# Kernel tuning notes

Measured on AMD Instinct MI355X. Metric: run time of the kernel, lower is better.

Reference implementation:

```python
import jax, jax.numpy as jnp
import numpy as np

B, R, L, K, E, H, V, QV = 256, 6, 10, 49, 300, 512, 2001, 10000


def _lstm_dir(x, Wih, Whh, bih, bhh):
    # x: [N, L, E]; returns final hidden state [N, H] (PyTorch gate order i,f,g,o)
    N = x.shape[0]
    Hd = Whh.shape[1]
    b = bih + bhh

    def step(carry, xt):
        h, c = carry
        gates = xt @ Wih.T + h @ Whh.T + b
        i, f, g, o = jnp.split(gates, 4, axis=-1)
        c = jax.nn.sigmoid(f) * c + jax.nn.sigmoid(i) * jnp.tanh(g)
        h = jax.nn.sigmoid(o) * jnp.tanh(c)
        return (h, c), None

    init = (jnp.zeros((N, Hd), x.dtype), jnp.zeros((N, Hd), x.dtype))
    (h, _), _ = jax.lax.scan(step, init, jnp.swapaxes(x, 0, 1))
    return h


def setup_inputs() -> dict:
    key = jax.random.key(0)
    ks = jax.random.split(key, 40)
    s = 0.02
    d = {}
    d['img'] = jax.random.normal(ks[0], (B * R, K, H), jnp.float32)
    d['role_qs'] = jax.random.randint(ks[1], (B, R, L), 0, QV, jnp.int64)
    d['qword_emb'] = jax.random.normal(ks[2], (QV, E), jnp.float32) * s
    d['lstm_Wih_f'] = jax.random.normal(ks[3], (4 * H, E), jnp.float32) * s
    d['lstm_Whh_f'] = jax.random.normal(ks[4], (4 * H, H), jnp.float32) * s
    d['lstm_bih_f'] = jnp.zeros((4 * H,), jnp.float32)
    d['lstm_bhh_f'] = jnp.zeros((4 * H,), jnp.float32)
    d['lstm_Wih_b'] = jax.random.normal(ks[5], (4 * H, E), jnp.float32) * s
    d['lstm_Whh_b'] = jax.random.normal(ks[6], (4 * H, H), jnp.float32) * s
    d['lstm_bih_b'] = jnp.zeros((4 * H,), jnp.float32)
    d['lstm_bhh_b'] = jnp.zeros((4 * H,), jnp.float32)
    d['proj_W'] = jax.random.normal(ks[7], (H, 2 * H), jnp.float32) * s
    d['proj_b'] = jnp.zeros((H,), jnp.float32)
    d['vatt_vW'] = jax.random.normal(ks[8], (H, H), jnp.float32) * s
    d['vatt_vb'] = jnp.zeros((H,), jnp.float32)
    d['vatt_qW'] = jax.random.normal(ks[9], (H, H), jnp.float32) * s
    d['vatt_qb'] = jnp.zeros((H,), jnp.float32)
    d['vatt_oW'] = jax.random.normal(ks[10], (1, H), jnp.float32) * s
    d['vatt_ob'] = jnp.zeros((1,), jnp.float32)
    d['qnet_W'] = jax.random.normal(ks[11], (H, H), jnp.float32) * s
    d['qnet_b'] = jnp.zeros((H,), jnp.float32)
    d['vnet_W'] = jax.random.normal(ks[12], (H, H), jnp.float32) * s
    d['vnet_b'] = jnp.zeros((H,), jnp.float32)
    d['cls_W1'] = jax.random.normal(ks[13], (2 * H, H), jnp.float32) * s
    d['cls_b1'] = jnp.zeros((2 * H,), jnp.float32)
    d['cls_W2'] = jax.random.normal(ks[14], (V, 2 * H), jnp.float32) * s
    d['cls_b2'] = jnp.zeros((V,), jnp.float32)
    d['g0_W'] = jax.random.normal(ks[15], (H, 2 * H), jnp.float32) * s
    d['g0_b'] = jnp.zeros((H,), jnp.float32)
    d['g1_W'] = jax.random.normal(ks[16], (H, H), jnp.float32) * s
    d['g1_b'] = jnp.zeros((H,), jnp.float32)
    d['g2_W'] = jax.random.normal(ks[17], (H, H), jnp.float32) * s
    d['g2_b'] = jnp.zeros((H,), jnp.float32)
    d['g3_W'] = jax.random.normal(ks[18], (H, H), jnp.float32) * s
    d['g3_b'] = jnp.zeros((H,), jnp.float32)
    d['f0_W'] = jax.random.normal(ks[19], (H, H), jnp.float32) * s
    d['f0_b'] = jnp.zeros((H,), jnp.float32)
    d['f1_W'] = jax.random.normal(ks[20], (H, H), jnp.float32) * s
    d['f1_b'] = jnp.zeros((H,), jnp.float32)
    return d


def _forward(img, qword_emb,
             lstm_Wih_f, lstm_Whh_f, lstm_bih_f, lstm_bhh_f,
             lstm_Wih_b, lstm_Whh_b, lstm_bih_b, lstm_bhh_b,
             proj_W, proj_b, vatt_vW, vatt_vb, vatt_qW, vatt_qb, vatt_oW, vatt_ob,
             qnet_W, qnet_b, vnet_W, vnet_b, cls_W1, cls_b1, cls_W2, cls_b2,
             g0_W, g0_b, g1_W, g1_b, g2_W, g2_b, g3_W, g3_b,
             f0_W, f0_b, f1_W, f1_b, role_qs):
    relu = jax.nn.relu
    bsz, roles = role_qs.shape[0], role_qs.shape[1]
    toks = role_qs.reshape(-1, role_qs.shape[-1])          # [B*R, L]
    w_emb = qword_emb[toks]                                 # [B*R, L, E]
    # bidirectional LSTM final hidden states
    h_f = _lstm_dir(w_emb, lstm_Wih_f, lstm_Whh_f, lstm_bih_f, lstm_bhh_f)
    h_b = _lstm_dir(w_emb[:, ::-1, :], lstm_Wih_b, lstm_Whh_b, lstm_bih_b, lstm_bhh_b)
    q_emb = jnp.concatenate([h_f, h_b], axis=-1) @ proj_W.T + proj_b   # [B*R, H]
    # top-down attention over image regions
    v_proj = relu(img @ vatt_vW.T + vatt_vb)                # [B*R, K, H]
    q_proj = relu(q_emb @ vatt_qW.T + vatt_qb)              # [B*R, H]
    att_logits = (v_proj * q_proj[:, None, :]) @ vatt_oW.T + vatt_ob  # [B*R, K, 1]
    att = jax.nn.softmax(att_logits, axis=1)
    v_emb = jnp.sum(att * img, axis=1)                      # [B*R, H]
    # joint representation + answer classifier
    q_repr = relu(q_emb @ qnet_W.T + qnet_b)
    v_repr = relu(v_emb @ vnet_W.T + vnet_b)
    joint_repr = q_repr * v_repr                            # [B*R, H]
    logits = relu(joint_repr @ cls_W1.T + cls_b1) @ cls_W2.T + cls_b2  # [B*R, V]
    # relation network over pairwise role representations
    jr = joint_repr.reshape(bsz, roles, -1)                 # [B, R, H]
    r1 = jnp.broadcast_to(jr[:, None, :, :], (bsz, roles, roles, jr.shape[-1]))
    r2 = jnp.broadcast_to(jr[:, :, None, :], (bsz, roles, roles, jr.shape[-1]))
    cat = jnp.concatenate([r1, r2], axis=-1).reshape(-1, 2 * jr.shape[-1])  # [B*R*R, 2H]
    g = relu(cat @ g0_W.T + g0_b)
    g = relu(g @ g1_W.T + g1_b)
    g = relu(g @ g2_W.T + g2_b)
    g = relu(g @ g3_W.T + g3_b)
    g = g.reshape(bsz, roles * roles, -1).sum(axis=1)       # [B, H]
    rec = relu(g @ f0_W.T + f0_b) @ f1_W.T + f1_b           # [B, H]
    rec = rec / jnp.sqrt(jnp.sum(rec * rec, axis=1, keepdims=True))  # l2norm
    return logits, rec


def reference(img, role_qs, qword_emb,
              lstm_Wih_f, lstm_Whh_f, lstm_bih_f, lstm_bhh_f,
              lstm_Wih_b, lstm_Whh_b, lstm_bih_b, lstm_bhh_b,
              proj_W, proj_b, vatt_vW, vatt_vb, vatt_qW, vatt_qb, vatt_oW, vatt_ob,
              qnet_W, qnet_b, vnet_W, vnet_b, cls_W1, cls_b1, cls_W2, cls_b2,
              g0_W, g0_b, g1_W, g1_b, g2_W, g2_b, g3_W, g3_b,
              f0_W, f0_b, f1_W, f1_b):
    return _forward(img, qword_emb,
                    lstm_Wih_f, lstm_Whh_f, lstm_bih_f, lstm_bhh_f,
                    lstm_Wih_b, lstm_Whh_b, lstm_bih_b, lstm_bhh_b,
                    proj_W, proj_b, vatt_vW, vatt_vb, vatt_qW, vatt_qb, vatt_oW, vatt_ob,
                    qnet_W, qnet_b, vnet_W, vnet_b, cls_W1, cls_b1, cls_W2, cls_b2,
                    g0_W, g0_b, g1_W, g1_b, g2_W, g2_b, g3_W, g3_b,
                    f0_W, f0_b, f1_W, f1_b, role_qs)
```

## Files before the change

### kernel.cpp

```cpp
#include <hip/hip_runtime.h>
#include <hip/hip_bf16.h>
#include <math.h>

typedef __attribute__((ext_vector_type(8))) short short8;
typedef __attribute__((ext_vector_type(4))) float f32x4;

#define KTILE 32
#define LSTR 40
#define LSTR64 72

__device__ __forceinline__ short8 cvt8(const float* x) {
    short8 r;
#pragma unroll
    for (int i = 0; i < 8; ++i) {
        __hip_bfloat16 b = __float2bfloat16(x[i]);
        r[i] = *reinterpret_cast<const short*>(&b);
    }
    return r;
}
__device__ __forceinline__ float bf2f(short s) {
    unsigned int u = ((unsigned int)(unsigned short)s) << 16;
    return __uint_as_float(u);
}

template<int BM>
__global__ __launch_bounds__(256)
void mfma_gemm_t(const float* __restrict__ A1f, int lda1, int k1,
                 const short* __restrict__ W1, int ldw1,
                 const float* __restrict__ A2f, int lda2, int k2,
                 const short* __restrict__ W2, int ldw2,
                 const float* __restrict__ bias1,
                 const float* __restrict__ mulvec, const float* __restrict__ mul,
                 float* __restrict__ C, int ldc, int M, int N,
                 int do_relu, int mode, int abits, int c_bf16)
{
    __shared__ short sA[2][BM][LSTR];
    __shared__ short sB[2][64][LSTR];
    __shared__ float sred[BM][2];
    constexpr int MF = BM / 32;

    const int tid = threadIdx.x;
    int m0, n0, ch8 = 0;
    if (mode == 1) {
        const int xcd = blockIdx.x & 7;
        const int gi = xcd * 588 + (blockIdx.x >> 3);
        m0 = (gi >> 3) << 7;
        ch8 = gi & 7;
        n0 = ch8 << 6;
    } else {
        m0 = blockIdx.y * BM;
        n0 = blockIdx.x << 6;
    }
    const short* A1b = (const short*)A1f;
    const short* A2b = (const short*)A2f;
    const int Ktot = k1 + k2;
// ... 134 lines not shown
                }
            }
        }
    } else {
#pragma unroll
        for (int m = 0; m < MF; ++m) {
#pragma unroll
            for (int j = 0; j < 4; ++j) {
                const int rloc = wr + (m << 4) + (lh << 2) + j;
                const int r = m0 + rloc;
                const size_t sqbase = (size_t)(r / 49) * ldc;
                float s = 0.f;
#pragma unroll
                for (int n = 0; n < 2; ++n) {
                    const int c = n0 + wc + (n << 4) + l15;
                    float v = acc[m][n][j] + bias1[c];
                    v = fmaxf(v, 0.f);
                    s += v * mul[sqbase + c];
                }
                s += __shfl_xor(s, 1, 64);
                s += __shfl_xor(s, 2, 64);
                s += __shfl_xor(s, 4, 64);
                s += __shfl_xor(s, 8, 64);
                if (l15 == 0) sred[rloc][wc >> 5] = s;
            }
        }
        __syncthreads();
        if (tid < BM)
            C[(size_t)(m0 + tid) * 8 + ch8] = sred[tid][0] + sred[tid][1];
    }
}

__global__ __launch_bounds__(256)
void mfma_gemm64_kernel(const float* __restrict__ A1f, int lda1, int k1,
                        const short* __restrict__ W1, int ldw1,
                        const float* __restrict__ A2f, int lda2, int k2,
                        const short* __restrict__ W2, int ldw2,
                        const float* __restrict__ bias1,
                        const float* __restrict__ mulvec, const float* __restrict__ mul,
                        float* __restrict__ C, int ldc, int M, int N,
                        int do_relu, int abits, int c_bf16)
{
    __shared__ short sA[2][64][LSTR64];
    __shared__ short sB[2][64][LSTR64];
    const int tid = threadIdx.x;
    const int m0 = blockIdx.y << 6, n0 = blockIdx.x << 6;
    const short* A1b = (const short*)A1f;
    const short* A2b = (const short*)A2f;
    const int Ktot = k1 + k2;
    const int nt = (Ktot + 63) >> 6;
    const int lane = tid & 63, wave = tid >> 6;
    const int wr = (wave >> 1) << 5, wc = (wave & 1) << 5;
    const int l15 = lane & 15, lh = lane >> 4;
    const int srow = tid >> 2, skq = (tid & 3) << 4;
    const int rgA = min(m0 + srow, M - 1);
    const int ngW = min(n0 + srow, N - 1);

    f32x4 acc[2][2];
#pragma unroll
    for (int m = 0; m < 2; ++m)
#pragma unroll
        for (int n = 0; n < 2; ++n) acc[m][n] = (f32x4){0.f, 0.f, 0.f, 0.f};

    short8 aS0, aS1, wS0, wS1;
    auto loadA = [&](int t) {
        const int k0 = (t << 6) + skq;
// ... 118 lines not shown
                 const float* __restrict__ vnet, const float* __restrict__ cls1,
                 const float* __restrict__ cls2, const float* __restrict__ g0,
                 const float* __restrict__ g1, const float* __restrict__ g2,
                 const float* __restrict__ g3, const float* __restrict__ f0,
                 const float* __restrict__ f1, short* __restrict__ dst)
{
    size_t idx = ((size_t)blockIdx.x * 256 + threadIdx.x) * 8;
    if (idx >= 5981184) return;
    const float* s;
    if (idx < 524288) s = proj + idx;
    else if (idx < 786432) s = qW + (idx - 524288);
    else if (idx < 1048576) s = vW + (idx - 786432);
    else if (idx < 1310720) s = qnet + (idx - 1048576);
    else if (idx < 1572864) s = vnet + (idx - 1310720);
    else if (idx < 2097152) s = cls1 + (idx - 1572864);
    else if (idx < 4146176) s = cls2 + (idx - 2097152);
    else if (idx < 4670464) {
        size_t li = idx - 4146176;
        int c = (int)(li >> 9), k = (int)(li & 511);
        s = (c < 512) ? g0 + (size_t)c * 1024 + k
                      : g0 + (size_t)(c - 512) * 1024 + 512 + k;
    }
    else if (idx < 4932608) s = g1 + (idx - 4670464);
    else if (idx < 5194752) s = g2 + (idx - 4932608);
    else if (idx < 5456896) s = g3 + (idx - 5194752);
    else if (idx < 5719040) s = f0 + (idx - 5456896);
    else s = f1 + (idx - 5719040);
    float4 a = *(const float4*)s, b = *(const float4*)(s + 4);
    float t[8] = {a.x, a.y, a.z, a.w, b.x, b.y, b.z, b.w};
    *(short8*)(dst + idx) = cvt8(t);
}

__global__ __launch_bounds__(256)
void lstm_reorder_kernel(const float* __restrict__ Wih, const float* __restrict__ Whh,
                         const float* __restrict__ bih, const float* __restrict__ bhh,
                         short* __restrict__ Wbf, float* __restrict__ bias_perm)
{
    int id = blockIdx.x * 256 + threadIdx.x;
    int c = id >> 9, k = id & 511;
    int src = (c & 3) * 512 + (c >> 2);
    {
        __hip_bfloat16 b = __float2bfloat16(Whh[(size_t)src * 512 + k]);
        Wbf[(size_t)c * 832 + k] = *(short*)&b;
    }
    if (k < 300) {
        __hip_bfloat16 b = __float2bfloat16(Wih[(size_t)src * 300 + k]);
        Wbf[(size_t)c * 832 + 512 + k] = *(short*)&b;
    } else if (k < 320) {
        Wbf[(size_t)c * 832 + 512 + k] = 0;
    }
    if (k == 0) bias_perm[c] = bih[src] + bhh[src];
}

__global__ __launch_bounds__(256)
void lstm_step4_kernel(const short* __restrict__ hF_in, const short* __restrict__ hB_in,
                       const short* __restrict__ WbfF, const short* __restrict__ WbfB,
                       const float* __restrict__ biasF, const float* __restrict__ biasB,
                       const float* __restrict__ emb, const int* __restrict__ toks,
                       int tF, int tB, int first,
                       short* __restrict__ hF_out, short* __restrict__ hB_out,
                       float* __restrict__ cF, float* __restrict__ cB)
{
    __shared__ short sA[2][64][LSTR64];
    __shared__ short sB[2][64][LSTR64];
    const int dir = blockIdx.z;
    const short* h_in = dir ? hB_in : hF_in;
    const short* Wbf  = dir ? WbfB : WbfF;
    const float* bias_perm = dir ? biasB : biasF;
    short* h_out  = dir ? hB_out : hF_out;
    float* cstate = dir ? cB : cF;
    const int tt = dir ? tB : tF;

    const int tid = threadIdx.x;
    const int m0 = blockIdx.y << 6;
    const int n0 = blockIdx.x << 6;
    const int lane = tid & 63, wave = tid >> 6;
    const int wr = (wave >> 1) << 5, wc = (wave & 1) << 5;
    const int l15 = lane & 15, lh = lane >> 4;
    const int srow = tid >> 2, skq = (tid & 3) << 4;
    const int rgA = m0 + srow;
    const int ngW = n0 + srow;
    const int nt = 13;
    const int arow = toks[rgA * 10 + tt];

    f32x4 acc[2][2];
#pragma unroll
    for (int m = 0; m < 2; ++m)
#pragma unroll
        for (int n = 0; n < 2; ++n) acc[m][n] = (f32x4){0.f, 0.f, 0.f, 0.f};

    short8 aS0, aS1, wS0, wS1;
    auto loadA = [&](int t) {
        const int k0 = (t << 6) + skq;
        if (k0 + 16 <= 512) {
            if (first) { short8 z = {0,0,0,0,0,0,0,0}; aS0 = z; aS1 = z; }
            else {
                const short* p = h_in + (size_t)rgA * 512 + k0;
                aS0 = *(const short8*)p; aS1 = *(const short8*)(p + 8);
            }
        } else if (k0 >= 512 && k0 + 16 <= 812) {
            const float* p = emb + (size_t)arow * 300 + (k0 - 512);
            float4 v0 = *(const float4*)p, v1 = *(const float4*)(p + 4);
            float4 v2 = *(const float4*)(p + 8), v3 = *(const float4*)(p + 12);
            float t0[8] = {v0.x, v0.y, v0.z, v0.w, v1.x, v1.y, v1.z, v1.w};
            float t1[8] = {v2.x, v2.y, v2.z, v2.w, v3.x, v3.y, v3.z, v3.w};
            aS0 = cvt8(t0); aS1 = cvt8(t1);
        } else {
            float tmp[16];
#pragma unroll
            for (int e = 0; e < 16; ++e) {
                const int kg = k0 + e;
                float v = 0.f;
                if (kg < 512) v = first ? 0.f : bf2f(h_in[(size_t)rgA * 512 + kg]);
                else if (kg < 812) v = emb[(size_t)arow * 300 + (kg - 512)];
                tmp[e] = v;
            }
            aS0 = cvt8(tmp); aS1 = cvt8(tmp + 8);
        }
    };
    auto loadW = [&](int t) {
        const short* p = Wbf + (size_t)ngW * 832 + (t << 6) + skq;
        wS0 = *(const short8*)p; wS1 = *(const short8*)(p + 8);
    };
    auto writeS = [&](int buf) {
        *(short8*)&sA[buf][srow][skq] = aS0;
        *(short8*)&sA[buf][srow][skq + 8] = aS1;
        *(short8*)&sB[buf][srow][skq] = wS0;
        *(short8*)&sB[buf][srow][skq + 8] = wS1;
    };

    loadA(0); loadW(0); writeS(0);
    __syncthreads();
    for (int t = 0; t < nt; ++t) {
        const int cur = t & 1;
        if (t + 1 < nt) { loadA(t + 1); loadW(t + 1); }
#pragma unroll
        for (int kk = 0; kk < 2; ++kk) {
            short8 af[2], bfv[2];
#pragma unroll
            for (int m = 0; m < 2; ++m)
                af[m] = *(const short8*)&sA[cur][wr + (m << 4) + l15][(kk << 5) + (lh << 3)];
#pragma unroll
            for (int n = 0; n < 2; ++n)
                bfv[n] = *(const short8*)&sB[cur][wc + (n << 4) + l15][(kk << 5) + (lh << 3)];
#pragma unroll
            for (int m = 0; m < 2; ++m)
#pragma unroll
                for (int n = 0; n < 2; ++n)
                    acc[m][n] = __builtin_amdgcn_mfma_f32_16x16x32_bf16(af[m], bfv[n], acc[m][n], 0, 0, 0);
        }
        if (t + 1 < nt) writeS(cur ^ 1);
        __syncthreads();
    }

#pragma unroll
    for (int n = 0; n < 2; ++n) {
        const int ccol = n0 + wc + (n << 4) + l15;
        const float bb = bias_perm[ccol];
        const int u = ccol >> 2;
#pragma unroll
        for (int m = 0; m < 2; ++m) {
#pragma unroll
            for (int j = 0; j < 4; ++j) {
                const int r = m0 + wr + (m << 4) + (lh << 2) + j;
                float v = acc[m][n][j] + bb;
                const int base = lane & ~3;
                float gi = __shfl(v, base, 64);
                float gf = __shfl(v, base | 1, 64);
                float gg = __shfl(v, base | 2, 64);
                float go = __shfl(v, base | 3, 64);
                if ((lane & 3) == 0) {
                    float si = 1.f / (1.f + expf(-gi));
                    float sf = 1.f / (1.f + expf(-gf));
                    float so = 1.f / (1.f + expf(-go));
                    size_t idx = ((size_t)r << 9) + u;
                    float cold = first ? 0.f : cstate[idx];
                    float cv = sf * cold + si * tanhf(gg);
                    cstate[idx] = cv;
                    float hv = so * tanhf(cv);
                    __hip_bfloat16 b = __float2bfloat16(hv);
                    h_out[idx] = *(short*)&b;
                }
            }
        }
    }
}

__global__ __launch_bounds__(256)
void imgcvt_kernel(const float* __restrict__ img, short* __restrict__ out)
{
    size_t i = ((size_t)blockIdx.x * 256 + threadIdx.x) * 8;
    float4 a = *(const float4*)(img + i), b = *(const float4*)(img + i + 4);
    float t[8] = {a.x, a.y, a.z, a.w, b.x, b.y, b.z, b.w};
    *(short8*)(out + i) = cvt8(t);
}

__global__ __launch_bounds__(256)
void attn_vemb_kernel(const float* __restrict__ partial, const float* __restrict__ img,
                      const short* __restrict__ imgb, float* __restrict__ v_emb)
{
    __shared__ float satt[49];
    const int n = blockIdx.x;
    const int tid = threadIdx.x;
    if (tid < 64) {
        float v = -1e30f;
        if (tid < 49) {
            const float* pp = partial + ((size_t)n * 49 + tid) * 8;
            v = ((pp[0] + pp[1]) + (pp[2] + pp[3])) + ((pp[4] + pp[5]) + (pp[6] + pp[7]));
        }
        float m = v;
#pragma unroll
        for (int off = 32; off; off >>= 1) m = fmaxf(m, __shfl_xor(m, off, 64));
        float e = (tid < 49) ? expf(v - m) : 0.f;
        float s = e;
// ... 103 lines not shown
    const float* cls_W2 = (const float*)d_in[25];
    const float* cls_b2 = (const float*)d_in[26];
    const float* g0_W   = (const float*)d_in[27];
    const float* g0_b   = (const float*)d_in[28];
    const float* g1_W   = (const float*)d_in[29];
    const float* g1_b   = (const float*)d_in[30];
    const float* g2_W   = (const float*)d_in[31];
    const float* g2_b   = (const float*)d_in[32];
    const float* g3_W   = (const float*)d_in[33];
    const float* g3_b   = (const float*)d_in[34];
    const float* f0_W   = (const float*)d_in[35];
    const float* f0_b   = (const float*)d_in[36];
    const float* f1_W   = (const float*)d_in[37];
    const float* f1_b   = (const float*)d_in[38];

    float* out_logits = (float*)d_out;
    float* out_rec    = (float*)d_out + 1536 * 2001;

    const size_t FB = 786432;
    float* zone = (float*)d_ws;
    float* gA    = zone;
    float* gB    = zone + 4718592;
    float* hid1  = zone + 9437184;
    float* PQb   = zone + 11010048;
    float* gsumb = zone + 12582912;
    float* f0o   = zone + 12713984;
    float* rectb = zone + 12845056;
    float* p = zone + 12976128;
    auto alloc = [&](size_t nf) { float* q = p; p += nf; return q; };
    float* hP0   = alloc(FB);
    float* hP2   = alloc(FB);
    float* joint = alloc(FB);
    float* partial = alloc(602112);
    short* WbfF  = (short*)alloc(851968);
    short* WbfB  = (short*)alloc(851968);
    float* biasF = alloc(2048);
    float* biasB = alloc(2048);
    const size_t TOPF = 17645568;
    short* wb = (short*)(zone + TOPF);
    short* projbf = wb;
    short* qWbf   = wb + 524288;
    short* vWbf   = wb + 786432;
    short* qnetbf = wb + 1048576;
    short* vnetbf = wb + 1310720;
    short* cls1bf = wb + 1572864;
    short* cls2bf = wb + 2097152;
    short* wpqbf  = wb + 4146176;
    short* g1bf   = wb + 4670464;
    short* g2bf   = wb + 4932608;
    short* g3bf   = wb + 5194752;
    short* f0bf   = wb + 5456896;
    short* f1bf   = wb + 5719040;
    const size_t WEND = TOPF + 2990592;
    const size_t IMGBF = 19267584;
    const bool useimgbf = ws_size >= (WEND + IMGBF) * sizeof(float);
    short* imgbf = (short*)(zone + WEND);
    short* hP1 = (short*)gA;
    short* hP3 = (short*)(gA + FB);
    float* cF  = gA + 2 * FB;
    float* cB  = gA + 3 * FB;
    float* q_emb  = PQb;
    float* swq    = hid1;
    float* q_repr = gA;
    float* v_emb  = gA + FB;

    auto gemm = [&](const float* A1, int lda1, int k1, const short* W1, int ldw1,
                    const float* A2, int lda2, int k2, const short* W2, int ldw2,
                    const float* b1, const float* mv, const float* mulp,
                    float* Cp, int ldc, int M, int N, int relu, int abits, int cbf) {
        if (M >= 4096) {
            dim3 g((N + 63) / 64, (M + 127) / 128);
            hipLaunchKernelGGL(HIP_KERNEL_NAME(mfma_gemm_t<128>), g, dim3(256), 0, stream,
                               A1, lda1, k1, W1, ldw1, A2, lda2, k2, W2, ldw2,
                               b1, mv, mulp, Cp, ldc, M, N, relu, 0, abits, cbf);
        } else {
            dim3 g((N + 63) / 64, (M + 63) / 64);
            hipLaunchKernelGGL(mfma_gemm64_kernel, g, dim3(256), 0, stream,
                               A1, lda1, k1, W1, ldw1, A2, lda2, k2, W2, ldw2,
                               b1, mv, mulp, Cp, ldc, M, N, relu, abits, cbf);
        }
    };

    const int NR = 1536;
    hipLaunchKernelGGL(lstm_reorder_kernel, dim3(4096), dim3(256), 0, stream,
                       Wih_f, Whh_f, bih_f, bhh_f, WbfF, biasF);
    hipLaunchKernelGGL(lstm_reorder_kernel, dim3(4096), dim3(256), 0, stream,
                       Wih_b, Whh_b, bih_b, bhh_b, WbfB, biasB);
    hipLaunchKernelGGL(wcvt_kernel, dim3(2921), dim3(256), 0, stream,
                       proj_W, vatt_qW, vatt_vW, qnet_W, vnet_W, cls_W1, cls_W2,
                       g0_W, g1_W, g2_W, g3_W, f0_W, f1_W, wb);
    if (useimgbf)
        hipLaunchKernelGGL(imgcvt_kernel, dim3(18816), dim3(256), 0, stream, img, imgbf);
    {
        short *fi = (short*)hP0, *fo = hP1, *bi = (short*)hP2, *bo = hP3;
        for (int t = 0; t < 10; ++t) {
            hipLaunchKernelGGL(lstm_step4_kernel, dim3(32, 24, 2), dim3(256), 0, stream,
                               fi, bi, WbfF, WbfB, biasF, biasB, qword, toks, t, 9 - t,
                               (t == 0) ? 1 : 0, fo, bo, cF, cB);
            short* tmp = fi; fi = fo; fo = tmp;
            tmp = bi; bi = bo; bo = tmp;
        }
    }

    gemm(hP0, 512, 512, projbf, 1024, hP2, 512, 512, projbf + 512, 1024,
         proj_b, nullptr, nullptr, q_emb, 512, NR, 512, 0, 3, 1);
    gemm(q_emb, 512, 512, qWbf, 512, nullptr, 0, 0, nullptr, 0,
         vatt_qb, vatt_oW, nullptr, swq, 512, NR, 512, 1, 1, 0);
    hipLaunchKernelGGL(HIP_KERNEL_NAME(mfma_gemm_t<128>), dim3(4704), dim3(256), 0, stream,
                       useimgbf ? (const float*)imgbf : img, 512, 512, vWbf, 512,
                       (const float*)nullptr, 0, 0, (const short*)nullptr, 0,
                       vatt_vb, (const float*)nullptr, swq,
                       partial, 512, 75264, 512, 0, 1, useimgbf ? 1 : 0, 0);
    hipLaunchKernelGGL(attn_vemb_kernel, dim3(1536), dim3(256), 0, stream,
                       partial, img, useimgbf ? imgbf : (const short*)nullptr, v_emb);
    gemm(q_emb, 512, 512, qnetbf, 512, nullptr, 0, 0, nullptr, 0,
         qnet_b, nullptr, nullptr, q_repr, 512, NR, 512, 1, 1, 0);
    gemm(v_emb, 512, 512, vnetbf, 512, nullptr, 0, 0, nullptr, 0,
         vnet_b, nullptr, q_repr, joint, 512, NR, 512, 1, 0, 1);
    gemm(joint, 512, 512, cls1bf, 512, nullptr, 0, 0, nullptr, 0,
         cls_b1, nullptr, nullptr, hid1, 1024, NR, 1024, 1, 1, 1);
    gemm(hid1, 1024, 1024, cls2bf, 1024, nullptr, 0, 0, nullptr, 0,
         cls_b2, nullptr, nullptr, out_logits, 2001, NR, 2001, 0, 1, 0);
    gemm(joint, 512, 512, wpqbf, 512, nullptr, 0, 0, nullptr, 0,
         nullptr, nullptr, nullptr, PQb, 1024, NR, 1024, 0, 1, 0);
    hipLaunchKernelGGL(g0build_kernel, dim3(18432), dim3(256), 0, stream,
                       PQb, g0_b, (short*)gA);
    gemm(gA, 512, 512, g1bf, 512, nullptr, 0, 0, nullptr, 0,
         g1_b, nullptr, nullptr, gB, 512, 9216, 512, 1, 1, 1);
    gemm(gB, 512, 512, g2bf, 512, nullptr, 0, 0, nullptr, 0,
         g2_b, nullptr, nullptr, gA, 512, 9216, 512, 1, 1, 1);
    gemm(gA, 512, 512, g3bf, 512, nullptr, 0, 0, nullptr, 0,
         g3_b, nullptr, nullptr, gB, 512, 9216, 512, 1, 1, 1);
    hipLaunchKernelGGL(gsum_kernel, dim3(512), dim3(256), 0, stream, (const short*)gB, gsumb);
    gemm(gsumb, 512, 512, f0bf, 512, nullptr, 0, 0, nullptr, 0,
         f0_b, nullptr, nullptr, f0o, 512, 256, 512, 1, 0, 0);
    gemm(f0o, 512, 512, f1bf, 512, nullptr, 0, 0, nullptr, 0,
         f1_b, nullptr, nullptr, rectb, 512, 256, 512, 0, 0, 0);
    hipLaunchKernelGGL(l2norm_kernel, dim3(256), dim3(256), 0, stream, rectb, out_rec);
}
```

Measured before the change: 828.5 us.

## Pre-swizzle LSTM weights into MFMA fragment layout and drop LDS staging

The LSTM weight reorder kernel now writes bf16 weights in the exact per-lane MFMA B-fragment order, so each wave reads its operand with one contiguous 16-byte load per lane. The step kernel drops the shared-memory double buffer and the barriers and loads A fragments (hidden state and embeddings) straight from global memory into registers. On the first step it skips the hidden-state half of K entirely. The trade-off is the loss of LDS reuse across waves: A rows are now loaded by two waves and W by two waves, and there is no software prefetch to hide global latency.

```diff
diff --git a/kernel.cpp b/kernel.cpp
--- a/kernel.cpp
+++ b/kernel.cpp
@@ -405,56 +405,57 @@
 }
 
 __global__ __launch_bounds__(256)
-void lstm_reorder_kernel(const float* __restrict__ Wih, const float* __restrict__ Whh,
-                         const float* __restrict__ bih, const float* __restrict__ bhh,
-                         short* __restrict__ Wbf, float* __restrict__ bias_perm)
+void lstm_reorder2_kernel(const float* __restrict__ Wih, const float* __restrict__ Whh,
+                          const float* __restrict__ bih, const float* __restrict__ bhh,
+                          short* __restrict__ WP, float* __restrict__ bias_perm)
 {
     int id = blockIdx.x * 256 + threadIdx.x;
-    int c = id >> 9, k = id & 511;
+    int c = id / 832, k = id % 832;
     int src = (c & 3) * 512 + (c >> 2);
-    {
-        __hip_bfloat16 b = __float2bfloat16(Whh[(size_t)src * 512 + k]);
-        Wbf[(size_t)c * 832 + k] = *(short*)&b;
-    }
-    if (k < 300) {
-        __hip_bfloat16 b = __float2bfloat16(Wih[(size_t)src * 300 + k]);
-        Wbf[(size_t)c * 832 + 512 + k] = *(short*)&b;
-    } else if (k < 320) {
-        Wbf[(size_t)c * 832 + 512 + k] = 0;
-    }
+    float v = 0.f;
+    if (k < 512) v = Whh[(size_t)src * 512 + k];
+    else if (k < 812) v = Wih[(size_t)src * 300 + (k - 512)];
+    __hip_bfloat16 b = __float2bfloat16(v);
+    const int cb = c >> 6, rem = c & 63;
+    const int wc2 = rem >> 5, n2 = (rem >> 4) & 1, l15 = rem & 15;
+    const int t = k >> 5, kk = k & 31;
+    const int lane = ((kk >> 3) << 4) + l15;
+    const int s = (cb * 2 + wc2) * 52 + t * 2 + n2;
+    WP[(size_t)s * 512 + lane * 8 + (kk & 7)] = *(short*)&b;
     if (k == 0) bias_perm[c] = bih[src] + bhh[src];
 }
 
 __global__ __launch_bounds__(256)
-void lstm_step4_kernel(const short* __restrict__ hF_in, const short* __restrict__ hB_in,
-                       const short* __restrict__ WbfF, const short* __restrict__ WbfB,
+void lstm_step5_kernel(const short* __restrict__ hF_in, const short* __restrict__ hB_in,
+                       const short* __restrict__ WPF, const short* __restrict__ WPB,
                        const float* __restrict__ biasF, const float* __restrict__ biasB,
                        const float* __restrict__ emb, const int* __restrict__ toks,
                        int tF, int tB, int first,
                        short* __restrict__ hF_out, short* __restrict__ hB_out,
                        float* __restrict__ cF, float* __restrict__ cB)
 {
-    __shared__ short sA[2][64][LSTR64];
-    __shared__ short sB[2][64][LSTR64];
     const int dir = blockIdx.z;
     const short* h_in = dir ? hB_in : hF_in;
-    const short* Wbf  = dir ? WbfB : WbfF;
+    const short* WP   = dir ? WPB : WPF;
     const float* bias_perm = dir ? biasB : biasF;
     short* h_out  = dir ? hB_out : hF_out;
     float* cstate = dir ? cB : cF;
     const int tt = dir ? tB : tF;
 
     const int tid = threadIdx.x;
+    const int lane = tid & 63, wave = tid >> 6;
+    const int cb = blockIdx.x;
     const int m0 = blockIdx.y << 6;
-    const int n0 = blockIdx.x << 6;
-    const int lane = tid & 63, wave = tid >> 6;
-    const int wr = (wave >> 1) << 5, wc = (wave & 1) << 5;
+    const int wr = (wave >> 1) << 5;
+    const int wc2 = wave & 1;
+    const int wc = wc2 << 5;
+    const int n0 = cb << 6;
     const int l15 = lane & 15, lh = lane >> 4;
-    const int srow = tid >> 2, skq = (tid & 3) << 4;
-    const int rgA = m0 + srow;
-    const int ngW = n0 + srow;
-    const int nt = 13;
-    const int arow = toks[rgA * 10 + tt];
+
+    const int row0 = m0 + wr + l15;
+    const int row1 = row0 + 16;
+    const int arow0 = toks[row0 * 10 + tt];
+    const int arow1 = toks[row1 * 10 + tt];
 
     f32x4 acc[2][2];
 #pragma unroll
@@ -462,68 +463,48 @@
 #pragma unroll
         for (int n = 0; n < 2; ++n) acc[m][n] = (f32x4){0.f, 0.f, 0.f, 0.f};
 
-    short8 aS0, aS1, wS0, wS1;
-    auto loadA = [&](int t) {
-        const int k0 = (t << 6) + skq;
-        if (k0 + 16 <= 512) {
-            if (first) { short8 z = {0,0,0,0,0,0,0,0}; aS0 = z; aS1 = z; }
-            else {
-                const short* p = h_in + (size_t)rgA * 512 + k0;
-                aS0 = *(const short8*)p; aS1 = *(const short8*)(p + 8);
-            }
-        } else if (k0 >= 512 && k0 + 16 <= 812) {
-            const float* p = emb + (size_t)arow * 300 + (k0 - 512);
-            float4 v0 = *(const float4*)p, v1 = *(const float4*)(p + 4);
-            float4 v2 = *(const float4*)(p + 8), v3 = *(const float4*)(p + 12);
-            float t0[8] = {v0.x, v0.y, v0.z, v0.w, v1.x, v1.y, v1.z, v1.w};
-            float t1[8] = {v2.x, v2.y, v2.z, v2.w, v3.x, v3.y, v3.z, v3.w};
-            aS0 = cvt8(t0); aS1 = cvt8(t1);
+    const short* wp = WP + ((size_t)(cb * 2 + wc2) * 52) * 512 + (lane << 3);
+
+    if (!first) {
+        for (int t = 0; t < 16; ++t) {
+            short8 af0 = *(const short8*)(h_in + (size_t)row0 * 512 + (t << 5) + (lh << 3));
+            short8 af1 = *(const short8*)(h_in + (size_t)row1 * 512 + (t << 5) + (lh << 3));
+            short8 bf0 = *(const short8*)(wp + (size_t)(t * 2) * 512);
+            short8 bf1 = *(const short8*)(wp + (size_t)(t * 2 + 1) * 512);
+            acc[0][0] = __builtin_amdgcn_mfma_f32_16x16x32_bf16(af0, bf0, acc[0][0], 0, 0, 0);
+            acc[0][1] = __builtin_amdgcn_mfma_f32_16x16x32_bf16(af0, bf1, acc[0][1], 0, 0, 0);
+            acc[1][0] = __builtin_amdgcn_mfma_f32_16x16x32_bf16(af1, bf0, acc[1][0], 0, 0, 0);
+            acc[1][1] = __builtin_amdgcn_mfma_f32_16x16x32_bf16(af1, bf1, acc[1][1], 0, 0, 0);
+        }
+    }
+    for (int t = 16; t < 26; ++t) {
+        const int c0 = (t << 5) + (lh << 3) - 512;
+        short8 af0, af1;
+        if (c0 + 8 <= 300) {
+            const float* p0 = emb + (size_t)arow0 * 300 + c0;
+            float4 u0 = *(const float4*)p0, u1 = *(const float4*)(p0 + 4);
+            float t0[8] = {u0.x, u0.y, u0.z, u0.w, u1.x, u1.y, u1.z, u1.w};
+            af0 = cvt8(t0);
+            const float* p1 = emb + (size_t)arow1 * 300 + c0;
+            float4 v0 = *(const float4*)p1, v1 = *(const float4*)(p1 + 4);
+            float t1[8] = {v0.x, v0.y, v0.z, v0.w, v1.x, v1.y, v1.z, v1.w};
+            af1 = cvt8(t1);
         } else {
-            float tmp[16];
-#pragma unroll
-            for (int e = 0; e < 16; ++e) {
-                const int kg = k0 + e;
-                float v = 0.f;
-                if (kg < 512) v = first ? 0.f : bf2f(h_in[(size_t)rgA * 512 + kg]);
-                else if (kg < 812) v = emb[(size_t)arow * 300 + (kg - 512)];
-                tmp[e] = v;
-            }
-            aS0 = cvt8(tmp); aS1 = cvt8(tmp + 8);
-        }
-    };
-    auto loadW = [&](int t) {
-        const short* p = Wbf + (size_t)ngW * 832 + (t << 6) + skq;
-        wS0 = *(const short8*)p; wS1 = *(const short8*)(p + 8);
-    };
-    auto writeS = [&](int buf) {
-        *(short8*)&sA[buf][srow][skq] = aS0;
-        *(short8*)&sA[buf][srow][skq + 8] = aS1;
-        *(short8*)&sB[buf][srow][skq] = wS0;
-        *(short8*)&sB[buf][srow][skq + 8] = wS1;
-    };
-
-    loadA(0); loadW(0); writeS(0);
-    __syncthreads();
-    for (int t = 0; t < nt; ++t) {
-        const int cur = t & 1;
-        if (t + 1 < nt) { loadA(t + 1); loadW(t + 1); }
-#pragma unroll
-        for (int kk = 0; kk < 2; ++kk) {
-            short8 af[2], bfv[2];
-#pragma unroll
-            for (int m = 0; m < 2; ++m)
-                af[m] = *(const short8*)&sA[cur][wr + (m << 4) + l15][(kk << 5) + (lh << 3)];
-#pragma unroll
-            for (int n = 0; n < 2; ++n)
-                bfv[n] = *(const short8*)&sB[cur][wc + (n << 4) + l15][(kk << 5) + (lh << 3)];
-#pragma unroll
-            for (int m = 0; m < 2; ++m)
-#pragma unroll
-                for (int n = 0; n < 2; ++n)
-                    acc[m][n] = __builtin_amdgcn_mfma_f32_16x16x32_bf16(af[m], bfv[n], acc[m][n], 0, 0, 0);
-        }
-        if (t + 1 < nt) writeS(cur ^ 1);
-        __syncthreads();
+            float t0[8], t1[8];
+#pragma unroll
+            for (int e = 0; e < 8; ++e) {
+                const int kg = c0 + e;
+                t0[e] = (kg < 300) ? emb[(size_t)arow0 * 300 + kg] : 0.f;
+                t1[e] = (kg < 300) ? emb[(size_t)arow1 * 300 + kg] : 0.f;
+            }
+            af0 = cvt8(t0); af1 = cvt8(t1);
+        }
+        short8 bf0 = *(const short8*)(wp + (size_t)(t * 2) * 512);
+        short8 bf1 = *(const short8*)(wp + (size_t)(t * 2 + 1) * 512);
+        acc[0][0] = __builtin_amdgcn_mfma_f32_16x16x32_bf16(af0, bf0, acc[0][0], 0, 0, 0);
+        acc[0][1] = __builtin_amdgcn_mfma_f32_16x16x32_bf16(af0, bf1, acc[0][1], 0, 0, 0);
+        acc[1][0] = __builtin_amdgcn_mfma_f32_16x16x32_bf16(af1, bf0, acc[1][0], 0, 0, 0);
+        acc[1][1] = __builtin_amdgcn_mfma_f32_16x16x32_bf16(af1, bf1, acc[1][1], 0, 0, 0);
     }
 
 #pragma unroll
@@ -722,8 +703,8 @@
     float* hP2   = alloc(FB);
     float* joint = alloc(FB);
     float* partial = alloc(602112);
-    short* WbfF  = (short*)alloc(851968);
-    short* WbfB  = (short*)alloc(851968);
+    short* WPF   = (short*)alloc(851968);
+    short* WPB   = (short*)alloc(851968);
     float* biasF = alloc(2048);
     float* biasB = alloc(2048);
     const size_t TOPF = 17645568;
@@ -772,10 +753,10 @@
     };
 
     const int NR = 1536;
-    hipLaunchKernelGGL(lstm_reorder_kernel, dim3(4096), dim3(256), 0, stream,
-                       Wih_f, Whh_f, bih_f, bhh_f, WbfF, biasF);
-    hipLaunchKernelGGL(lstm_reorder_kernel, dim3(4096), dim3(256), 0, stream,
-                       Wih_b, Whh_b, bih_b, bhh_b, WbfB, biasB);
+    hipLaunchKernelGGL(lstm_reorder2_kernel, dim3(6656), dim3(256), 0, stream,
+                       Wih_f, Whh_f, bih_f, bhh_f, WPF, biasF);
+    hipLaunchKernelGGL(lstm_reorder2_kernel, dim3(6656), dim3(256), 0, stream,
+                       Wih_b, Whh_b, bih_b, bhh_b, WPB, biasB);
     hipLaunchKernelGGL(wcvt_kernel, dim3(2921), dim3(256), 0, stream,
                        proj_W, vatt_qW, vatt_vW, qnet_W, vnet_W, cls_W1, cls_W2,
                        g0_W, g1_W, g2_W, g3_W, f0_W, f1_W, wb);
@@ -784,8 +765,8 @@
     {
         short *fi = (short*)hP0, *fo = hP1, *bi = (short*)hP2, *bo = hP3;
         for (int t = 0; t < 10; ++t) {
-            hipLaunchKernelGGL(lstm_step4_kernel, dim3(32, 24, 2), dim3(256), 0, stream,
-                               fi, bi, WbfF, WbfB, biasF, biasB, qword, toks, t, 9 - t,
+            hipLaunchKernelGGL(lstm_step5_kernel, dim3(32, 24, 2), dim3(256), 0, stream,
+                               fi, bi, WPF, WPB, biasF, biasB, qword, toks, t, 9 - t,
                                (t == 0) ? 1 : 0, fo, bo, cF, cB);
             short* tmp = fi; fi = fo; fo = tmp;
             tmp = bi; bi = bo; bo = tmp;
```

Result: slower. 1.014 ms (+22.3%).

## Fuse ten LSTM step launches into one persistent cooperative kernel with grid sync

Applied to the files above, without the earlier changes.

Replaces the per-timestep launches of the bidirectional LSTM step kernel with a single cooperative kernel of 1536 blocks that loops over the ten steps and separates them with grid.sync(). The aim is to remove repeated kernel launch overhead and the gaps between steps. In exchange it pays for a grid-wide barrier at each step and needs every block resident at once. The occupancy check falls back to the old launch loop when that cannot be met. Final hidden states end in the same buffers (step 9 writes hFb, the same buffer as the old hP1).

```diff
diff --git a/kernel.cpp b/kernel.cpp
--- a/kernel.cpp
+++ b/kernel.cpp
@@ -1,6 +1,9 @@
 #include <hip/hip_runtime.h>
 #include <hip/hip_bf16.h>
+#include <hip/hip_cooperative_groups.h>
 #include <math.h>
+
+namespace cg = cooperative_groups;
 
 typedef __attribute__((ext_vector_type(8))) short short8;
 typedef __attribute__((ext_vector_type(4))) float f32x4;
@@ -553,6 +556,136 @@
                     float hv = so * tanhf(cv);
                     __hip_bfloat16 b = __float2bfloat16(hv);
                     h_out[idx] = *(short*)&b;
+                }
+            }
+        }
+    }
+}
+
+__global__ __launch_bounds__(256)
+void lstm_persist_kernel(short* hFa, short* hFb, short* hBa, short* hBb,
+                         const short* __restrict__ WbfF, const short* __restrict__ WbfB,
+                         const float* __restrict__ biasF, const float* __restrict__ biasB,
+                         const float* __restrict__ emb, const int* __restrict__ toks,
+                         float* __restrict__ cF, float* __restrict__ cB)
+{
+    cg::grid_group grid = cg::this_grid();
+    __shared__ short sA[2][64][LSTR];
+    __shared__ short sB[2][64][LSTR];
+    const int bid = blockIdx.x;
+    const int dir = bid >= 768;
+    const int g = bid - (dir ? 768 : 0);
+    const int cb = g & 31, rb = g >> 5;
+    const short* Wbf = dir ? WbfB : WbfF;
+    const float* bias_perm = dir ? biasB : biasF;
+    float* cstate = dir ? cB : cF;
+    short* hb0 = dir ? hBa : hFa;
+    short* hb1 = dir ? hBb : hFb;
+
+    const int tid = threadIdx.x;
+    const int m0 = rb << 6, n0 = cb << 6;
+    const int lane = tid & 63, wave = tid >> 6;
+    const int wr = (wave >> 1) << 5, wc = (wave & 1) << 5;
+    const int l15 = lane & 15, lh = lane >> 4;
+    const int srow = tid >> 2, skq = (tid & 3) << 3;
+    const int rgA = m0 + srow;
+    const int ngW = n0 + srow;
+
+    for (int step = 0; step < 10; ++step) {
+        if (step) grid.sync();
+        const int tt = dir ? (9 - step) : step;
+        const int first = (step == 0);
+        const short* h_in = (step & 1) ? hb1 : hb0;
+        short* h_out = (step & 1) ? hb0 : hb1;
+        const int arow = toks[rgA * 10 + tt];
+
+        f32x4 acc[2][2];
+#pragma unroll
+        for (int m = 0; m < 2; ++m)
+#pragma unroll
+            for (int n = 0; n < 2; ++n) acc[m][n] = (f32x4){0.f, 0.f, 0.f, 0.f};
+
+        short8 aS, wS;
+        auto loadA = [&](int t) {
+            const int k0 = (t << 5) + skq;
+            if (k0 + 8 <= 512) {
+                if (first) { short8 z = {0,0,0,0,0,0,0,0}; aS = z; }
+                else aS = *(const short8*)(h_in + (size_t)rgA * 512 + k0);
+            } else if (k0 >= 512 && k0 + 8 <= 812) {
+                const float* p = emb + (size_t)arow * 300 + (k0 - 512);
+                float4 v0 = *(const float4*)p, v1 = *(const float4*)(p + 4);
+                float t0[8] = {v0.x, v0.y, v0.z, v0.w, v1.x, v1.y, v1.z, v1.w};
+                aS = cvt8(t0);
+            } else {
+                float tmp[8];
+#pragma unroll
+                for (int e = 0; e < 8; ++e) {
+                    const int kg = k0 + e;
+                    float v = 0.f;
+                    if (kg < 512) v = first ? 0.f : bf2f(h_in[(size_t)rgA * 512 + kg]);
+                    else if (kg < 812) v = emb[(size_t)arow * 300 + (kg - 512)];
+                    tmp[e] = v;
+                }
+                aS = cvt8(tmp);
+            }
+        };
+        auto loadW = [&](int t) {
+            wS = *(const short8*)&Wbf[(size_t)ngW * 832 + (t << 5) + skq];
+        };
+        auto writeS = [&](int buf) {
+            *(short8*)&sA[buf][srow][skq] = aS;
+            *(short8*)&sB[buf][srow][skq] = wS;
+        };
+
+        loadA(0); loadW(0); writeS(0);
+        __syncthreads();
+        for (int t = 0; t < 26; ++t) {
+            const int cur = t & 1;
+            if (t + 1 < 26) { loadA(t + 1); loadW(t + 1); }
+            short8 af[2], bfv[2];
+#pragma unroll
+            for (int m = 0; m < 2; ++m)
+                af[m] = *(const short8*)&sA[cur][wr + (m << 4) + l15][lh << 3];
+#pragma unroll
+            for (int n = 0; n < 2; ++n)
+                bfv[n] = *(const short8*)&sB[cur][wc + (n << 4) + l15][lh << 3];
+#pragma unroll
+            for (int m = 0; m < 2; ++m)
+#pragma unroll
+                for (int n = 0; n < 2; ++n)
+                    acc[m][n] = __builtin_amdgcn_mfma_f32_16x16x32_bf16(af[m], bfv[n], acc[m][n], 0, 0, 0);
+            if (t + 1 < 26) writeS(cur ^ 1);
+            __syncthreads();
+        }
+
+#pragma unroll
+        for (int n = 0; n < 2; ++n) {
+            const int ccol = n0 + wc + (n << 4) + l15;
+            const float bb = bias_perm[ccol];
+            const int u = ccol >> 2;
+#pragma unroll
+            for (int m = 0; m < 2; ++m) {
+#pragma unroll
+                for (int j = 0; j < 4; ++j) {
+                    const int r = m0 + wr + (m << 4) + (lh << 2) + j;
+                    float v = acc[m][n][j] + bb;
+                    const int base = lane & ~3;
+                    float gi = __shfl(v, base, 64);
+                    float gf = __shfl(v, base | 1, 64);
+                    float gg = __shfl(v, base | 2, 64);
+                    float go = __shfl(v, base | 3, 64);
+                    if ((lane & 3) == 0) {
+                        float si = 1.f / (1.f + expf(-gi));
+                        float sf = 1.f / (1.f + expf(-gf));
+                        float so = 1.f / (1.f + expf(-go));
+                        size_t idx = ((size_t)r << 9) + u;
+                        float cold = first ? 0.f : cstate[idx];
+                        float cv = sf * cold + si * tanhf(gg);
+                        cstate[idx] = cv;
+                        float hv = so * tanhf(cv);
+                        __hip_bfloat16 b = __float2bfloat16(hv);
+                        h_out[idx] = *(short*)&b;
+                    }
                 }
             }
         }
@@ -781,14 +914,34 @@
                        g0_W, g1_W, g2_W, g3_W, f0_W, f1_W, wb);
     if (useimgbf)
         hipLaunchKernelGGL(imgcvt_kernel, dim3(18816), dim3(256), 0, stream, img, imgbf);
+
     {
-        short *fi = (short*)hP0, *fo = hP1, *bi = (short*)hP2, *bo = hP3;
-        for (int t = 0; t < 10; ++t) {
-            hipLaunchKernelGGL(lstm_step4_kernel, dim3(32, 24, 2), dim3(256), 0, stream,
-                               fi, bi, WbfF, WbfB, biasF, biasB, qword, toks, t, 9 - t,
-                               (t == 0) ? 1 : 0, fo, bo, cF, cB);
-            short* tmp = fi; fi = fo; fo = tmp;
-            tmp = bi; bi = bo; bo = tmp;
+        bool coop = false;
+        int maxb = 0;
+        hipError_t oe = hipOccupancyMaxActiveBlocksPerMultiprocessor(
+            &maxb, reinterpret_cast<const void*>(lstm_persist_kernel), 256, 0);
+        if (oe == hipSuccess && maxb >= 6) {
+            short* a0 = (short*)hP0; short* a1 = hP1;
+            short* b0 = (short*)hP2; short* b1 = hP3;
+            const short* wf = WbfF; const short* wbk = WbfB;
+            const float* bf_ = biasF; const float* bb_ = biasB;
+            const float* em = qword; const int* tk = toks;
+            float* cf_ = cF; float* cb_ = cB;
+            void* args[] = {&a0, &a1, &b0, &b1, &wf, &wbk, &bf_, &bb_, &em, &tk, &cf_, &cb_};
+            hipError_t e = hipLaunchCooperativeKernel(
+                reinterpret_cast<void*>(lstm_persist_kernel),
+                dim3(1536), dim3(256), args, 0, stream);
+            coop = (e == hipSuccess);
+        }
+        if (!coop) {
+            short *fi = (short*)hP0, *fo = hP1, *bi = (short*)hP2, *bo = hP3;
+            for (int t = 0; t < 10; ++t) {
+                hipLaunchKernelGGL(lstm_step4_kernel, dim3(32, 24, 2), dim3(256), 0, stream,
+                                   fi, bi, WbfF, WbfB, biasF, biasB, qword, toks, t, 9 - t,
+                                   (t == 0) ? 1 : 0, fo, bo, cF, cB);
+                short* tmp = fi; fi = fo; fo = tmp;
+                tmp = bi; bi = bo; bo = tmp;
+            }
         }
     }
 
```

New measurement: 826.3 us. No clear change (-0.3%).

## Use direct global-to-LDS loads with XOR swizzle for LSTM and attention GEMMs

Applied to the files above, without the earlier changes.

Adds a global_load_lds helper and two new kernels: an attention-logit GEMM that streams bf16 image and weight tiles straight into swizzled LDS, and an LSTM step kernel that does the same, with the embedding table pre-converted to padded bf16. Both still fuse their epilogues (attention logit reduction, and the gate math that updates c and h). The goal is to skip register staging and bank conflicts on the tile loads and to drop per-step fp32 embedding conversion. In exchange it needs extra workspace for the bf16 embedding table, an extra conversion kernel and two memsets, and it falls back to the old kernels when workspace is short.

```diff
diff --git a/kernel.cpp b/kernel.cpp
--- a/kernel.cpp
+++ b/kernel.cpp
@@ -21,6 +21,11 @@
 __device__ __forceinline__ float bf2f(short s) {
     unsigned int u = ((unsigned int)(unsigned short)s) << 16;
     return __uint_as_float(u);
+}
+__device__ __forceinline__ void gload16(const void* g, void* l) {
+    __builtin_amdgcn_global_load_lds(
+        (const __attribute__((address_space(1))) unsigned int*)g,
+        (__attribute__((address_space(3))) unsigned int*)l, 16, 0, 0);
 }
 
 template<int BM>
@@ -221,6 +226,100 @@
 }
 
 __global__ __launch_bounds__(256)
+void attn_logits3_kernel(const short* __restrict__ imgb, const short* __restrict__ vW,
+                         const float* __restrict__ vb, const float* __restrict__ swq,
+                         float* __restrict__ partial)
+{
+    __shared__ short sA[2][128][64];
+    __shared__ short sB[2][64][64];
+    __shared__ float sred[128][2];
+    const int tid = threadIdx.x;
+    const int lane = tid & 63, wave = tid >> 6;
+    const int xcd = blockIdx.x & 7;
+    const int gi = xcd * 588 + (blockIdx.x >> 3);
+    const int m0 = (gi >> 3) << 7;
+    const int ch8 = gi & 7;
+    const int n0 = ch8 << 6;
+    const int wr = (wave >> 1) << 6;
+    const int wc = (wave & 1) << 5;
+    const int l15 = lane & 15, lh = lane >> 4;
+    const int lr = lane >> 3;
+    const int sc = (lane & 7) ^ lr;
+
+    f32x4 acc[4][2];
+#pragma unroll
+    for (int m = 0; m < 4; ++m)
+#pragma unroll
+        for (int n = 0; n < 2; ++n) acc[m][n] = (f32x4){0.f, 0.f, 0.f, 0.f};
+
+    auto stage = [&](int t, int buf) {
+        const int kb = t << 6;
+#pragma unroll
+        for (int j = 0; j < 4; ++j) {
+            const int r0 = (wave << 5) + (j << 3);
+            const int grow = m0 + r0 + lr;
+            gload16(imgb + (size_t)grow * 512 + kb + (sc << 3), &sA[buf][r0][0]);
+        }
+#pragma unroll
+        for (int j = 0; j < 2; ++j) {
+            const int r0 = (wave << 4) + (j << 3);
+            const int grow = n0 + r0 + lr;
+            gload16(vW + (size_t)grow * 512 + kb + (sc << 3), &sB[buf][r0][0]);
+        }
+    };
+
+    stage(0, 0);
+    __syncthreads();
+    for (int t = 0; t < 8; ++t) {
+        const int cur = t & 1;
+        if (t + 1 < 8) stage(t + 1, cur ^ 1);
+#pragma unroll
+        for (int kk = 0; kk < 2; ++kk) {
+            const int rd = (((kk << 2) + lh) ^ (l15 & 7)) << 3;
+            short8 af[4], bfv[2];
+#pragma unroll
+            for (int m = 0; m < 4; ++m)
+                af[m] = *(const short8*)&sA[cur][wr + (m << 4) + l15][rd];
+#pragma unroll
+            for (int n = 0; n < 2; ++n)
+                bfv[n] = *(const short8*)&sB[cur][wc + (n << 4) + l15][rd];
+#pragma unroll
+            for (int m = 0; m < 4; ++m)
+#pragma unroll
+                for (int n = 0; n < 2; ++n)
+                    acc[m][n] = __builtin_amdgcn_mfma_f32_16x16x32_bf16(af[m], bfv[n], acc[m][n], 0, 0, 0);
+        }
+        __syncthreads();
+    }
+
+#pragma unroll
+    for (int m = 0; m < 4; ++m) {
+#pragma unroll
+        for (int j = 0; j < 4; ++j) {
+            const int rloc = wr + (m << 4) + (lh << 2) + j;
+            const int r = m0 + rloc;
+            const size_t sqbase = (size_t)(r / 49) * 512;
+            float s = 0.f;
+#pragma unroll
+            for (int n = 0; n < 2; ++n) {
+                const int c = n0 + wc + (n << 4) + l15;
+                float v = acc[m][n][j] + vb[c];
+                v = fmaxf(v, 0.f);
+                s += v * swq[sqbase + c];
+            }
+            s += __shfl_xor(s, 1, 64);
+            s += __shfl_xor(s, 2, 64);
+            s += __shfl_xor(s, 4, 64);
+            s += __shfl_xor(s, 8, 64);
+            if (l15 == 0) sred[rloc][wc >> 5] = s;
+        }
+    }
+    __syncthreads();
+    if (tid < 128)
+        partial[(size_t)(m0 + tid) * 8 + ch8] = sred[tid][0] + sred[tid][1];
+}
+
+__global__ __launch_bounds__(256)
 void mfma_gemm64_kernel(const float* __restrict__ A1f, int lda1, int k1,
                         const short* __restrict__ W1, int ldw1,
                         const float* __restrict__ A2f, int lda2, int k2,
@@ -423,6 +522,130 @@
         Wbf[(size_t)c * 832 + 512 + k] = 0;
     }
     if (k == 0) bias_perm[c] = bih[src] + bhh[src];
+}
+
+__global__ __launch_bounds__(256)
+void embcvt_kernel(const float* __restrict__ qword, short* __restrict__ embp)
+{
+    int id = blockIdx.x * 256 + threadIdx.x;
+    if (id >= 3200000) return;
+    int r = id / 320, c = id % 320;
+    float v = (c < 300) ? qword[(size_t)r * 300 + c] : 0.f;
+    __hip_bfloat16 b = __float2bfloat16(v);
+    embp[id] = *(short*)&b;
+}
+
+__global__ __launch_bounds__(256)
+void lstm_step6_kernel(const short* __restrict__ hF_in, const short* __restrict__ hB_in,
+                       const short* __restrict__ WbfF, const short* __restrict__ WbfB,
+                       const float* __restrict__ biasF, const float* __restrict__ biasB,
+                       const short* __restrict__ embp, const int* __restrict__ toks,
+                       int tF, int tB, int first,
+                       short* __restrict__ hF_out, short* __restrict__ hB_out,
+                       float* __restrict__ cF, float* __restrict__ cB)
+{
+    __shared__ short sA[2][64][64];
+    __shared__ short sB[2][64][64];
+    const int dir = blockIdx.z;
+    const short* h_in = dir ? hB_in : hF_in;
+    const short* Wbf  = dir ? WbfB : WbfF;
+    const float* bias_perm = dir ? biasB : biasF;
+    short* h_out  = dir ? hB_out : hF_out;
+    float* cstate = dir ? cB : cF;
+    const int tt = dir ? tB : tF;
+
+    const int tid = threadIdx.x;
+    const int m0 = blockIdx.y << 6;
+    const int n0 = blockIdx.x << 6;
+    const int lane = tid & 63, wave = tid >> 6;
+    const int wr = (wave >> 1) << 5, wc = (wave & 1) << 5;
+    const int l15 = lane & 15, lh = lane >> 4;
+    const int lr = lane >> 3;
+    const int sc = (lane & 7) ^ lr;
+
+    f32x4 acc[2][2];
+#pragma unroll
+    for (int m = 0; m < 2; ++m)
+#pragma unroll
+        for (int n = 0; n < 2; ++n) acc[m][n] = (f32x4){0.f, 0.f, 0.f, 0.f};
+
+    auto stage = [&](int t, int buf) {
+#pragma unroll
+        for (int j = 0; j < 2; ++j) {
+            const int r0 = (wave << 4) + (j << 3);
+            const int grow = m0 + r0 + lr;
+            const short* g;
+            if (t < 8) {
+                g = h_in + (size_t)grow * 512 + (t << 6) + (sc << 3);
+            } else {
+                const int ar = toks[grow * 10 + tt];
+                g = embp + (size_t)ar * 320 + ((t - 8) << 6) + (sc << 3);
+            }
+            gload16(g, &sA[buf][r0][0]);
+        }
+#pragma unroll
+        for (int j = 0; j < 2; ++j) {
+            const int r0 = (wave << 4) + (j << 3);
+            const int grow = n0 + r0 + lr;
+            gload16(Wbf + (size_t)grow * 832 + (t << 6) + (sc << 3), &sB[buf][r0][0]);
+        }
+    };
+
+    stage(0, 0);
+    __syncthreads();
+    for (int t = 0; t < 13; ++t) {
+        const int cur = t & 1;
+        if (t + 1 < 13) stage(t + 1, cur ^ 1);
+#pragma unroll
+        for (int kk = 0; kk < 2; ++kk) {
+            const int rd = (((kk << 2) + lh) ^ (l15 & 7)) << 3;
+            short8 af[2], bfv[2];
+#pragma unroll
+            for (int m = 0; m < 2; ++m)
+                af[m] = *(const short8*)&sA[cur][wr + (m << 4) + l15][rd];
+#pragma unroll
+            for (int n = 0; n < 2; ++n)
+                bfv[n] = *(const short8*)&sB[cur][wc + (n << 4) + l15][rd];
+#pragma unroll
+            for (int m = 0; m < 2; ++m)
+#pragma unroll
+                for (int n = 0; n < 2; ++n)
+                    acc[m][n] = __builtin_amdgcn_mfma_f32_16x16x32_bf16(af[m], bfv[n], acc[m][n], 0, 0, 0);
+        }
+        __syncthreads();
+    }
+
+#pragma unroll
+    for (int n = 0; n < 2; ++n) {
+        const int ccol = n0 + wc + (n << 4) + l15;
+        const float bb = bias_perm[ccol];
+        const int u = ccol >> 2;
+#pragma unroll
+        for (int m = 0; m < 2; ++m) {
+#pragma unroll
+            for (int j = 0; j < 4; ++j) {
+                const int r = m0 + wr + (m << 4) + (lh << 2) + j;
+                float v = acc[m][n][j] + bb;
+                const int base = lane & ~3;
+                float gi = __shfl(v, base, 64);
+                float gf = __shfl(v, base | 1, 64);
+                float gg = __shfl(v, base | 2, 64);
+                float go = __shfl(v, base | 3, 64);
+                if ((lane & 3) == 0) {
+                    float si = 1.f / (1.f + expf(-gi));
+                    float sf = 1.f / (1.f + expf(-gf));
+                    float so = 1.f / (1.f + expf(-go));
+                    size_t idx = ((size_t)r << 9) + u;
+                    float cold = first ? 0.f : cstate[idx];
+                    float cv = sf * cold + si * tanhf(gg);
+                    cstate[idx] = cv;
+                    float hv = so * tanhf(cv);
+                    __hip_bfloat16 b = __float2bfloat16(hv);
+                    h_out[idx] = *(short*)&b;
+                }
+            }
+        }
+    }
 }
 
 __global__ __launch_bounds__(256)
@@ -743,8 +966,11 @@
     short* f1bf   = wb + 5719040;
     const size_t WEND = TOPF + 2990592;
     const size_t IMGBF = 19267584;
+    const size_t EMBPF = 1600000;
     const bool useimgbf = ws_size >= (WEND + IMGBF) * sizeof(float);
+    const bool useglds  = ws_size >= (WEND + IMGBF + EMBPF) * sizeof(float);
     short* imgbf = (short*)(zone + WEND);
+    short* embp  = (short*)(zone + WEND + IMGBF);
     short* hP1 = (short*)gA;
     short* hP3 = (short*)(gA + FB);
     float* cF  = gA + 2 * FB;
@@ -781,7 +1007,20 @@
                        g0_W, g1_W, g2_W, g3_W, f0_W, f1_W, wb);
     if (useimgbf)
         hipLaunchKernelGGL(imgcvt_kernel, dim3(18816), dim3(256), 0, stream, img, imgbf);
-    {
+
+    if (useglds) {
+        hipLaunchKernelGGL(embcvt_kernel, dim3(12500), dim3(256), 0, stream, qword, embp);
+        hipMemsetAsync(hP0, 0, FB * sizeof(short), stream);
+        hipMemsetAsync(hP2, 0, FB * sizeof(short), stream);
+        short *fi = (short*)hP0, *fo = hP1, *bi = (short*)hP2, *bo = hP3;
+        for (int t = 0; t < 10; ++t) {
+            hipLaunchKernelGGL(lstm_step6_kernel, dim3(32, 24, 2), dim3(256), 0, stream,
+                               fi, bi, WbfF, WbfB, biasF, biasB, embp, toks, t, 9 - t,
+                               (t == 0) ? 1 : 0, fo, bo, cF, cB);
+            short* tmp = fi; fi = fo; fo = tmp;
+            tmp = bi; bi = bo; bo = tmp;
+        }
+    } else {
         short *fi = (short*)hP0, *fo = hP1, *bi = (short*)hP2, *bo = hP3;
         for (int t = 0; t < 10; ++t) {
             hipLaunchKernelGGL(lstm_step4_kernel, dim3(32, 24, 2), dim3(256), 0, stream,
@@ -796,11 +1035,16 @@
          proj_b, nullptr, nullptr, q_emb, 512, NR, 512, 0, 3, 1);
     gemm(q_emb, 512, 512, qWbf, 512, nullptr, 0, 0, nullptr, 0,
          vatt_qb, vatt_oW, nullptr, swq, 512, NR, 512, 1, 1, 0);
-    hipLaunchKernelGGL(HIP_KERNEL_NAME(mfma_gemm_t<128>), dim3(4704), dim3(256), 0, stream,
-                       useimgbf ? (const float*)imgbf : img, 512, 512, vWbf, 512,
-                       (const float*)nullptr, 0, 0, (const short*)nullptr, 0,
-                       vatt_vb, (const float*)nullptr, swq,
-                       partial, 512, 75264, 512, 0, 1, useimgbf ? 1 : 0, 0);
+    if (useimgbf) {
+        hipLaunchKernelGGL(attn_logits3_kernel, dim3(4704), dim3(256), 0, stream,
+                           imgbf, vWbf, vatt_vb, swq, partial);
+    } else {
+        hipLaunchKernelGGL(HIP_KERNEL_NAME(mfma_gemm_t<128>), dim3(4704), dim3(256), 0, stream,
+                           img, 512, 512, vWbf, 512,
+                           (const float*)nullptr, 0, 0, (const short*)nullptr, 0,
+                           vatt_vb, (const float*)nullptr, swq,
+                           partial, 512, 75264, 512, 0, 1, 0, 0);
+    }
     hipLaunchKernelGGL(attn_vemb_kernel, dim3(1536), dim3(256), 0, stream,
                        partial, img, useimgbf ? imgbf : (const short*)nullptr, v_emb);
     gemm(q_emb, 512, 512, qnetbf, 512, nullptr, 0, 0, nullptr, 0,
```

Result: faster. 787.5 us (-5.0%).
